# Kernel optimization log

Hardware: AMD Instinct MI355X
Metric: run time of the kernel (lower is better)

Reference implementation:

```python
import jax, jax.numpy as jnp
import numpy as np

EPS = 1e-5


def _grid_sample_bilinear(feats, grid):
    """PyTorch F.grid_sample, mode='bilinear', padding_mode='zeros', align_corners=False.
    feats: (BN, C, H, W); grid: (BN, Q, 2) with (x, y) in [-1, 1]. Returns (BN, C, Q)."""
    BN, C, H, W = feats.shape
    # unnormalize (align_corners=False): pix = ((g + 1) * size - 1) / 2
    x = ((grid[..., 0] + 1.0) * W - 1.0) * 0.5
    y = ((grid[..., 1] + 1.0) * H - 1.0) * 0.5
    x0f = jnp.floor(x)
    y0f = jnp.floor(y)
    wx = x - x0f  # fractional weights
    wy = y - y0f
    x0 = x0f.astype(jnp.int32)
    y0 = y0f.astype(jnp.int32)
    feats_flat = feats.reshape(BN, C, H * W)

    def corner(ix, iy, w):
        valid = (ix >= 0) & (ix < W) & (iy >= 0) & (iy < H)
        lin = jnp.clip(iy, 0, H - 1) * W + jnp.clip(ix, 0, W - 1)  # (BN, Q)
        g = jnp.take_along_axis(feats_flat, lin[:, None, :], axis=2)  # (BN, C, Q)
        return g * (w * valid)[:, None, :]

    return (corner(x0, y0, (1.0 - wx) * (1.0 - wy))
            + corner(x0 + 1, y0, wx * (1.0 - wy))
            + corner(x0, y0 + 1, (1.0 - wx) * wy)
            + corner(x0 + 1, y0 + 1, wx * wy))


def reference(query, reference_points, image_features, lidar2img, W_out, b_out):
    B, Q, _ = reference_points.shape
    N = lidar2img.shape[1]
    _, _, C, H, W = image_features.shape

    # --- project_3d_to_2d ---
    pts = jnp.broadcast_to(reference_points[:, None], (B, N, Q, 3))
    homo = jnp.concatenate([pts, jnp.ones_like(pts[..., :1])], axis=-1)  # (B,N,Q,4)
    p2h = jnp.einsum('bnij,bnqj->bnqi', lidar2img, homo)  # (B,N,Q,4)
    z = p2h[..., 2:3]
    points_2d = p2h[..., 0:2] / (jnp.abs(z) + EPS)
    front_mask = (z > EPS)[..., 0]  # (B,N,Q)

    # --- feature_sampling ---
    gx = points_2d[..., 0] / (W - 1) * 2.0 - 1.0
    gy = points_2d[..., 1] / (H - 1) * 2.0 - 1.0
    grid = jnp.stack([gx, gy], axis=-1)  # (B,N,Q,2)
    sampled = _grid_sample_bilinear(
        image_features.reshape(B * N, C, H, W), grid.reshape(B * N, Q, 2))  # (BN,C,Q)
    sampled = sampled.reshape(B, N, C, Q).transpose(0, 3, 1, 2)  # (B,Q,N,C)

    in_image = jnp.maximum(jnp.abs(gx), jnp.abs(gy)) <= 1.0  # (B,N,Q)
    valid = (front_mask & in_image).transpose(0, 2, 1)[..., None]  # (B,Q,N,1)
    sampled = sampled * valid

    # --- aggregate over cameras + output projection (dropout = identity in eval) ---
    agg = sampled.mean(axis=2)  # (B,Q,C)
    return agg @ W_out.T + b_out


def setup_inputs() -> dict:
    key = jax.random.key(0)
    ks = jax.random.split(key, 5)
    B, N, Q, C, H, W = 2, 6, 900, 256, 116, 200
    query = jax.random.normal(ks[0], (B, Q, C), jnp.float32)
    reference_points = jax.random.uniform(ks[1], (B, Q, 3), dtype=jnp.float32)
    image_features = jax.random.normal(ks[2], (B, N, C, H, W), jnp.float32)
    # scale rows so projections land around the image plane with mostly positive depth
    raw = jax.random.uniform(ks[3], (B, N, 4, 4), dtype=jnp.float32)
    row_scale = jnp.array([float(W), float(H), 2.0, 1.0], jnp.float32)[None, None, :, None]
    lidar2img = raw * row_scale
    W_out = jax.random.normal(ks[4], (C, C), jnp.float32) / np.sqrt(C).astype(np.float32)
    b_out = jnp.zeros((C,), jnp.float32)
    return {"query": query, "reference_points": reference_points,
            "image_features": image_features, "lidar2img": lidar2img,
            "W_out": W_out, "b_out": b_out}
```

## Files before the change

### kernel.cpp

```cpp
#include <hip/hip_runtime.h>
#include <hip/hip_bf16.h>
#include <cstdint>

#define Bb 2
#define Nc 6
#define Qn 900
#define Cc 256
#define Hc 116
#define Wc 200
#define EPSf 1e-5f

struct Proj { int x0, y0; float wx, wy; };

__global__ void proj_kernel(const float* __restrict__ ref_pts,
                            const float* __restrict__ l2i,
                            Proj* __restrict__ proj) {
    int t = blockIdx.x * blockDim.x + threadIdx.x;
    if (t >= Bb * Nc * Qn) return;
    int q  = t % Qn;
    int bn = t / Qn;
    int b  = bn / Nc;

    const float* p = ref_pts + ((size_t)b * Qn + q) * 3;
    float px = p[0], py = p[1], pz = p[2];
    const float* M = l2i + (size_t)bn * 16;
    float h0 = M[0]*px + M[1]*py + M[2]*pz  + M[3];
    float h1 = M[4]*px + M[5]*py + M[6]*pz  + M[7];
    float h2 = M[8]*px + M[9]*py + M[10]*pz + M[11];

    float denom = fabsf(h2) + EPSf;
    float x2d = h0 / denom;
    float y2d = h1 / denom;
    float gx = x2d / (float)(Wc - 1) * 2.0f - 1.0f;
    float gy = y2d / (float)(Hc - 1) * 2.0f - 1.0f;
    bool front = h2 > EPSf;
    bool in_img = fmaxf(fabsf(gx), fabsf(gy)) <= 1.0f;

    Proj o;
    if (front && in_img) {
        float x = ((gx + 1.0f) * (float)Wc - 1.0f) * 0.5f;
        float y = ((gy + 1.0f) * (float)Hc - 1.0f) * 0.5f;
        float x0f = floorf(x), y0f = floorf(y);
        o.x0 = (int)x0f;
        o.y0 = (int)y0f;
        o.wx = x - x0f;
        o.wy = y - y0f;
    } else {
        o.x0 = INT32_MIN; o.y0 = 0; o.wx = 0.0f; o.wy = 0.0f;
    }
    proj[t] = o;
}

__global__ void sample_kernel(const float* __restrict__ feats,
                              const Proj* __restrict__ proj,
                              float* __restrict__ agg) {
    int bq = blockIdx.x;
    int b  = bq / Qn;
    int q  = bq % Qn;
    int c  = threadIdx.x;

    float acc = 0.0f;
    #pragma unroll
    for (int n = 0; n < Nc; ++n) {
        int bn = b * Nc + n;
        Proj pr = proj[(size_t)bn * Qn + q];
        if (pr.x0 == INT32_MIN) continue;

        const float* img = feats + ((size_t)bn * Cc + c) * (size_t)(Hc * Wc);
        int x0 = pr.x0, y0 = pr.y0, x1 = x0 + 1, y1 = y0 + 1;
        float wx = pr.wx, wy = pr.wy;

        bool vx0 = (x0 >= 0) & (x0 < Wc);
        bool vx1 = (x1 >= 0) & (x1 < Wc);
        bool vy0 = (y0 >= 0) & (y0 < Hc);
        bool vy1 = (y1 >= 0) & (y1 < Hc);
        int cx0 = min(max(x0, 0), Wc - 1);
        int cx1 = min(max(x1, 0), Wc - 1);
        int cy0 = min(max(y0, 0), Hc - 1);
        int cy1 = min(max(y1, 0), Hc - 1);

        float v00 = img[cy0 * Wc + cx0] * ((vx0 & vy0) ? 1.0f : 0.0f);
        float v01 = img[cy0 * Wc + cx1] * ((vx1 & vy0) ? 1.0f : 0.0f);
        float v10 = img[cy1 * Wc + cx0] * ((vx0 & vy1) ? 1.0f : 0.0f);
        float v11 = img[cy1 * Wc + cx1] * ((vx1 & vy1) ? 1.0f : 0.0f);

        acc += (v00 * (1.0f - wx) + v01 * wx) * (1.0f - wy)
             + (v10 * (1.0f - wx) + v11 * wx) * wy;
    }
    agg[(size_t)bq * Cc + c] = acc * (1.0f / 6.0f);
}

#define QT 8
__global__ void out_gemm(const float* __restrict__ agg,
                         const float* __restrict__ Wm,
                         const float* __restrict__ bias,
                         float* __restrict__ out) {
    __shared__ float sA[QT][Cc];
    int base_q = blockIdx.x * QT;
    int tid = threadIdx.x;

    for (int i = tid; i < QT * Cc; i += 256)
        sA[i / Cc][i % Cc] = agg[(size_t)base_q * Cc + i];
    __syncthreads();

    float acc[QT];
    #pragma unroll
    for (int j = 0; j < QT; ++j) acc[j] = 0.0f;

    const float4* wrow = (const float4*)(Wm + (size_t)tid * Cc);
    #pragma unroll 4
    for (int c4 = 0; c4 < Cc / 4; ++c4) {
        float4 w = wrow[c4];
        #pragma unroll
        for (int j = 0; j < QT; ++j) {
            acc[j] += w.x * sA[j][4*c4 + 0] + w.y * sA[j][4*c4 + 1]
                    + w.z * sA[j][4*c4 + 2] + w.w * sA[j][4*c4 + 3];
        }
    }
    float bb = bias[tid];
    #pragma unroll
    for (int j = 0; j < QT; ++j)
        out[(size_t)(base_q + j) * Cc + tid] = acc[j] + bb;
}

extern "C" void kernel_launch(void* const* d_in, const int* in_sizes, int n_in,
                              void* d_out, int out_size, void* d_ws, size_t ws_size,
                              hipStream_t stream) {
    const float* ref_pts = (const float*)d_in[1];
    const float* feats   = (const float*)d_in[2];
    const float* l2i     = (const float*)d_in[3];
    const float* Wm      = (const float*)d_in[4];
    const float* bias    = (const float*)d_in[5];
    float* out = (float*)d_out;

    size_t proj_bytes = (size_t)Bb * Nc * Qn * sizeof(Proj);
    proj_bytes = (proj_bytes + 255) & ~(size_t)255;
    Proj*  proj = (Proj*)d_ws;
    float* agg  = (float*)((char*)d_ws + proj_bytes);

    int npts = Bb * Nc * Qn;
    proj_kernel<<<(npts + 255) / 256, 256, 0, stream>>>(ref_pts, l2i, proj);
    sample_kernel<<<Bb * Qn, 256, 0, stream>>>(feats, proj, agg);
    out_gemm<<<(Bb * Qn) / QT, 256, 0, stream>>>(agg, Wm, bias, out);
}
```

Before: 398.4 us.

## Transpose image features to channel-last bf16 and fuse projection into sampling

```diff
diff --git a/kernel.cpp b/kernel.cpp
--- a/kernel.cpp
+++ b/kernel.cpp
@@ -8,67 +8,92 @@
 #define Cc 256
 #define Hc 116
 #define Wc 200
+#define HWp (Hc * Wc)
+#define PT 32
+#define PTILES (HWp / PT)
 #define EPSf 1e-5f
 
-struct Proj { int x0, y0; float wx, wy; };
-
-__global__ void proj_kernel(const float* __restrict__ ref_pts,
-                            const float* __restrict__ l2i,
-                            Proj* __restrict__ proj) {
-    int t = blockIdx.x * blockDim.x + threadIdx.x;
-    if (t >= Bb * Nc * Qn) return;
-    int q  = t % Qn;
-    int bn = t / Qn;
-    int b  = bn / Nc;
-
-    const float* p = ref_pts + ((size_t)b * Qn + q) * 3;
-    float px = p[0], py = p[1], pz = p[2];
-    const float* M = l2i + (size_t)bn * 16;
-    float h0 = M[0]*px + M[1]*py + M[2]*pz  + M[3];
-    float h1 = M[4]*px + M[5]*py + M[6]*pz  + M[7];
-    float h2 = M[8]*px + M[9]*py + M[10]*pz + M[11];
-
-    float denom = fabsf(h2) + EPSf;
-    float x2d = h0 / denom;
-    float y2d = h1 / denom;
-    float gx = x2d / (float)(Wc - 1) * 2.0f - 1.0f;
-    float gy = y2d / (float)(Hc - 1) * 2.0f - 1.0f;
-    bool front = h2 > EPSf;
-    bool in_img = fmaxf(fabsf(gx), fabsf(gy)) <= 1.0f;
-
-    Proj o;
-    if (front && in_img) {
-        float x = ((gx + 1.0f) * (float)Wc - 1.0f) * 0.5f;
-        float y = ((gy + 1.0f) * (float)Hc - 1.0f) * 0.5f;
-        float x0f = floorf(x), y0f = floorf(y);
-        o.x0 = (int)x0f;
-        o.y0 = (int)y0f;
-        o.wx = x - x0f;
-        o.wy = y - y0f;
-    } else {
-        o.x0 = INT32_MIN; o.y0 = 0; o.wx = 0.0f; o.wy = 0.0f;
-    }
-    proj[t] = o;
+__device__ __forceinline__ unsigned short f2bf(float f) {
+    uint32_t u = __float_as_uint(f);
+    uint32_t r = (u + 0x7FFFu + ((u >> 16) & 1u)) >> 16;
+    return (unsigned short)r;
+}
+__device__ __forceinline__ float bf2f(unsigned short h) {
+    return __uint_as_float(((uint32_t)h) << 16);
 }
 
-__global__ void sample_kernel(const float* __restrict__ feats,
-                              const Proj* __restrict__ proj,
+__global__ void transpose_kernel(const float* __restrict__ in,
+                                 unsigned short* __restrict__ out) {
+    __shared__ float tile[PT][Cc + 1];
+    int blk = blockIdx.x;
+    int bn  = blk / PTILES;
+    int p0  = (blk % PTILES) * PT;
+    int tid = threadIdx.x;
+
+    const float* src = in + (size_t)bn * Cc * HWp + p0;
+    int pq = tid & 7;
+    int cb = tid >> 3;
+    #pragma unroll
+    for (int k = 0; k < 8; ++k) {
+        int c = cb + 32 * k;
+        float4 v = *(const float4*)(src + (size_t)c * HWp + 4 * pq);
+        tile[4 * pq + 0][c] = v.x;
+        tile[4 * pq + 1][c] = v.y;
+        tile[4 * pq + 2][c] = v.z;
+        tile[4 * pq + 3][c] = v.w;
+    }
+    __syncthreads();
+
+    int c4 = (tid & 63) * 4;
+    int pw = tid >> 6;
+    #pragma unroll
+    for (int j = 0; j < 8; ++j) {
+        int p = pw + 4 * j;
+        ushort4 u;
+        u.x = f2bf(tile[p][c4 + 0]);
+        u.y = f2bf(tile[p][c4 + 1]);
+        u.z = f2bf(tile[p][c4 + 2]);
+        u.w = f2bf(tile[p][c4 + 3]);
+        unsigned short* orow = out + ((size_t)bn * HWp + p0 + p) * Cc;
+        *(ushort4*)(orow + c4) = u;
+    }
+}
+
+__global__ void sample_kernel(const unsigned short* __restrict__ trans,
+                              const float* __restrict__ ref_pts,
+                              const float* __restrict__ l2i,
                               float* __restrict__ agg) {
     int bq = blockIdx.x;
     int b  = bq / Qn;
     int q  = bq % Qn;
     int c  = threadIdx.x;
 
+    const float* p = ref_pts + ((size_t)b * Qn + q) * 3;
+    float px = p[0], py = p[1], pz = p[2];
+
     float acc = 0.0f;
-    #pragma unroll
     for (int n = 0; n < Nc; ++n) {
         int bn = b * Nc + n;
-        Proj pr = proj[(size_t)bn * Qn + q];
-        if (pr.x0 == INT32_MIN) continue;
+        const float* M = l2i + (size_t)bn * 16;
+        float h0 = M[0] * px + M[1] * py + M[2]  * pz + M[3];
+        float h1 = M[4] * px + M[5] * py + M[6]  * pz + M[7];
+        float h2 = M[8] * px + M[9] * py + M[10] * pz + M[11];
 
-        const float* img = feats + ((size_t)bn * Cc + c) * (size_t)(Hc * Wc);
-        int x0 = pr.x0, y0 = pr.y0, x1 = x0 + 1, y1 = y0 + 1;
-        float wx = pr.wx, wy = pr.wy;
+        float denom = fabsf(h2) + EPSf;
+        float x2d = h0 / denom;
+        float y2d = h1 / denom;
+        float gx = x2d / (float)(Wc - 1) * 2.0f - 1.0f;
+        float gy = y2d / (float)(Hc - 1) * 2.0f - 1.0f;
+        bool front  = h2 > EPSf;
+        bool in_img = fmaxf(fabsf(gx), fabsf(gy)) <= 1.0f;
+        if (!(front && in_img)) continue;
+
+        float x = ((gx + 1.0f) * (float)Wc - 1.0f) * 0.5f;
+        float y = ((gy + 1.0f) * (float)Hc - 1.0f) * 0.5f;
+        float x0f = floorf(x), y0f = floorf(y);
+        int x0 = (int)x0f, y0 = (int)y0f;
+        int x1 = x0 + 1,  y1 = y0 + 1;
+        float wx = x - x0f, wy = y - y0f;
 
         bool vx0 = (x0 >= 0) & (x0 < Wc);
         bool vx1 = (x1 >= 0) & (x1 < Wc);
@@ -79,10 +104,11 @@
         int cy0 = min(max(y0, 0), Hc - 1);
         int cy1 = min(max(y1, 0), Hc - 1);
 
-        float v00 = img[cy0 * Wc + cx0] * ((vx0 & vy0) ? 1.0f : 0.0f);
-        float v01 = img[cy0 * Wc + cx1] * ((vx1 & vy0) ? 1.0f : 0.0f);
-        float v10 = img[cy1 * Wc + cx0] * ((vx0 & vy1) ? 1.0f : 0.0f);
-        float v11 = img[cy1 * Wc + cx1] * ((vx1 & vy1) ? 1.0f : 0.0f);
+        const unsigned short* base = trans + (size_t)bn * HWp * Cc;
+        float v00 = bf2f(base[(size_t)(cy0 * Wc + cx0) * Cc + c]) * ((vx0 & vy0) ? 1.0f : 0.0f);
+        float v01 = bf2f(base[(size_t)(cy0 * Wc + cx1) * Cc + c]) * ((vx1 & vy0) ? 1.0f : 0.0f);
+        float v10 = bf2f(base[(size_t)(cy1 * Wc + cx0) * Cc + c]) * ((vx0 & vy1) ? 1.0f : 0.0f);
+        float v11 = bf2f(base[(size_t)(cy1 * Wc + cx1) * Cc + c]) * ((vx1 & vy1) ? 1.0f : 0.0f);
 
         acc += (v00 * (1.0f - wx) + v01 * wx) * (1.0f - wy)
              + (v10 * (1.0f - wx) + v11 * wx) * wy;
@@ -113,8 +139,8 @@
         float4 w = wrow[c4];
         #pragma unroll
         for (int j = 0; j < QT; ++j) {
-            acc[j] += w.x * sA[j][4*c4 + 0] + w.y * sA[j][4*c4 + 1]
-                    + w.z * sA[j][4*c4 + 2] + w.w * sA[j][4*c4 + 3];
+            acc[j] += w.x * sA[j][4 * c4 + 0] + w.y * sA[j][4 * c4 + 1]
+                    + w.z * sA[j][4 * c4 + 2] + w.w * sA[j][4 * c4 + 3];
         }
     }
     float bb = bias[tid];
@@ -133,13 +159,11 @@
     const float* bias    = (const float*)d_in[5];
     float* out = (float*)d_out;
 
-    size_t proj_bytes = (size_t)Bb * Nc * Qn * sizeof(Proj);
-    proj_bytes = (proj_bytes + 255) & ~(size_t)255;
-    Proj*  proj = (Proj*)d_ws;
-    float* agg  = (float*)((char*)d_ws + proj_bytes);
+    size_t trans_bytes = (size_t)Bb * Nc * HWp * Cc * sizeof(unsigned short);
+    unsigned short* trans = (unsigned short*)d_ws;
+    float* agg = (float*)((char*)d_ws + trans_bytes);
 
-    int npts = Bb * Nc * Qn;
-    proj_kernel<<<(npts + 255) / 256, 256, 0, stream>>>(ref_pts, l2i, proj);
-    sample_kernel<<<Bb * Qn, 256, 0, stream>>>(feats, proj, agg);
+    transpose_kernel<<<Bb * Nc * PTILES, 256, 0, stream>>>(feats, trans);
+    sample_kernel<<<Bb * Qn, 256, 0, stream>>>(trans, ref_pts, l2i, agg);
     out_gemm<<<(Bb * Qn) / QT, 256, 0, stream>>>(agg, Wm, bias, out);
 }
```

Result: slower. 436.1 us (+9.5%).

## Sample from per-channel image planes staged in LDS as bf16 with atomic accumulation

Applied to the files above, without the earlier changes.

```diff
diff --git a/kernel.cpp b/kernel.cpp
--- a/kernel.cpp
+++ b/kernel.cpp
@@ -8,9 +8,19 @@
 #define Cc 256
 #define Hc 116
 #define Wc 200
+#define HWp (Hc * Wc)
 #define EPSf 1e-5f
 
 struct Proj { int x0, y0; float wx, wy; };
+
+__device__ __forceinline__ unsigned short f2bf(float f) {
+    uint32_t u = __float_as_uint(f);
+    uint32_t r = (u + 0x7FFFu + ((u >> 16) & 1u)) >> 16;
+    return (unsigned short)r;
+}
+__device__ __forceinline__ float bf2f(unsigned short h) {
+    return __uint_as_float(((uint32_t)h) << 16);
+}
 
 __global__ void proj_kernel(const float* __restrict__ ref_pts,
                             const float* __restrict__ l2i,
@@ -33,7 +43,7 @@
     float y2d = h1 / denom;
     float gx = x2d / (float)(Wc - 1) * 2.0f - 1.0f;
     float gy = y2d / (float)(Hc - 1) * 2.0f - 1.0f;
-    bool front = h2 > EPSf;
+    bool front  = h2 > EPSf;
     bool in_img = fmaxf(fabsf(gx), fabsf(gy)) <= 1.0f;
 
     Proj o;
@@ -41,32 +51,37 @@
         float x = ((gx + 1.0f) * (float)Wc - 1.0f) * 0.5f;
         float y = ((gy + 1.0f) * (float)Hc - 1.0f) * 0.5f;
         float x0f = floorf(x), y0f = floorf(y);
-        o.x0 = (int)x0f;
-        o.y0 = (int)y0f;
-        o.wx = x - x0f;
-        o.wy = y - y0f;
+        o.x0 = (int)x0f;  o.y0 = (int)y0f;
+        o.wx = x - x0f;   o.wy = y - y0f;
     } else {
         o.x0 = INT32_MIN; o.y0 = 0; o.wx = 0.0f; o.wy = 0.0f;
     }
     proj[t] = o;
 }
 
-__global__ void sample_kernel(const float* __restrict__ feats,
-                              const Proj* __restrict__ proj,
-                              float* __restrict__ agg) {
-    int bq = blockIdx.x;
-    int b  = bq / Qn;
-    int q  = bq % Qn;
-    int c  = threadIdx.x;
+__global__ __launch_bounds__(256) void plane_sample(const float* __restrict__ feats,
+                                                    const Proj* __restrict__ proj,
+                                                    float* __restrict__ agg) {
+    __shared__ unsigned short pl[HWp];
+    int blk = blockIdx.x;
+    int c  = blk & (Cc - 1);
+    int bn = blk >> 8;
+    int b  = bn / Nc;
 
-    float acc = 0.0f;
-    #pragma unroll
-    for (int n = 0; n < Nc; ++n) {
-        int bn = b * Nc + n;
-        Proj pr = proj[(size_t)bn * Qn + q];
+    const float4* src = (const float4*)(feats + ((size_t)bn * Cc + c) * (size_t)HWp);
+    #pragma unroll 1
+    for (int i = threadIdx.x; i < HWp / 4; i += 256) {
+        float4 v = src[i];
+        ushort4 u;
+        u.x = f2bf(v.x); u.y = f2bf(v.y); u.z = f2bf(v.z); u.w = f2bf(v.w);
+        ((ushort4*)pl)[i] = u;
+    }
+    __syncthreads();
+
+    const Proj* prow = proj + (size_t)bn * Qn;
+    for (int q = threadIdx.x; q < Qn; q += 256) {
+        Proj pr = prow[q];
         if (pr.x0 == INT32_MIN) continue;
-
-        const float* img = feats + ((size_t)bn * Cc + c) * (size_t)(Hc * Wc);
         int x0 = pr.x0, y0 = pr.y0, x1 = x0 + 1, y1 = y0 + 1;
         float wx = pr.wx, wy = pr.wy;
 
@@ -79,15 +94,15 @@
         int cy0 = min(max(y0, 0), Hc - 1);
         int cy1 = min(max(y1, 0), Hc - 1);
 
-        float v00 = img[cy0 * Wc + cx0] * ((vx0 & vy0) ? 1.0f : 0.0f);
-        float v01 = img[cy0 * Wc + cx1] * ((vx1 & vy0) ? 1.0f : 0.0f);
-        float v10 = img[cy1 * Wc + cx0] * ((vx0 & vy1) ? 1.0f : 0.0f);
-        float v11 = img[cy1 * Wc + cx1] * ((vx1 & vy1) ? 1.0f : 0.0f);
+        float v00 = bf2f(pl[cy0 * Wc + cx0]) * ((vx0 & vy0) ? 1.0f : 0.0f);
+        float v01 = bf2f(pl[cy0 * Wc + cx1]) * ((vx1 & vy0) ? 1.0f : 0.0f);
+        float v10 = bf2f(pl[cy1 * Wc + cx0]) * ((vx0 & vy1) ? 1.0f : 0.0f);
+        float v11 = bf2f(pl[cy1 * Wc + cx1]) * ((vx1 & vy1) ? 1.0f : 0.0f);
 
-        acc += (v00 * (1.0f - wx) + v01 * wx) * (1.0f - wy)
-             + (v10 * (1.0f - wx) + v11 * wx) * wy;
+        float val = (v00 * (1.0f - wx) + v01 * wx) * (1.0f - wy)
+                  + (v10 * (1.0f - wx) + v11 * wx) * wy;
+        atomicAdd(&agg[((size_t)b * Qn + q) * Cc + c], val);
     }
-    agg[(size_t)bq * Cc + c] = acc * (1.0f / 6.0f);
 }
 
 #define QT 8
@@ -100,7 +115,7 @@
     int tid = threadIdx.x;
 
     for (int i = tid; i < QT * Cc; i += 256)
-        sA[i / Cc][i % Cc] = agg[(size_t)base_q * Cc + i];
+        sA[i / Cc][i % Cc] = agg[(size_t)base_q * Cc + i] * (1.0f / 6.0f);
     __syncthreads();
 
     float acc[QT];
@@ -113,8 +128,8 @@
         float4 w = wrow[c4];
         #pragma unroll
         for (int j = 0; j < QT; ++j) {
-            acc[j] += w.x * sA[j][4*c4 + 0] + w.y * sA[j][4*c4 + 1]
-                    + w.z * sA[j][4*c4 + 2] + w.w * sA[j][4*c4 + 3];
+            acc[j] += w.x * sA[j][4 * c4 + 0] + w.y * sA[j][4 * c4 + 1]
+                    + w.z * sA[j][4 * c4 + 2] + w.w * sA[j][4 * c4 + 3];
         }
     }
     float bb = bias[tid];
@@ -137,9 +152,12 @@
     proj_bytes = (proj_bytes + 255) & ~(size_t)255;
     Proj*  proj = (Proj*)d_ws;
     float* agg  = (float*)((char*)d_ws + proj_bytes);
+    size_t agg_bytes = (size_t)Bb * Qn * Cc * sizeof(float);
+
+    hipMemsetAsync(agg, 0, agg_bytes, stream);
 
     int npts = Bb * Nc * Qn;
     proj_kernel<<<(npts + 255) / 256, 256, 0, stream>>>(ref_pts, l2i, proj);
-    sample_kernel<<<Bb * Qn, 256, 0, stream>>>(feats, proj, agg);
+    plane_sample<<<Bb * Nc * Cc, 256, 0, stream>>>(feats, proj, agg);
     out_gemm<<<(Bb * Qn) / QT, 256, 0, stream>>>(agg, Wm, bias, out);
 }
```

Result: slower. 488.1 us (+22.5%).
